# Kernel tuning notes

Measured on AMD Instinct MI355X. Metric: run time of the kernel, lower is better.

## Reference

```python
import jax, jax.numpy as jnp
import numpy as np

ALPHA = 0.2  # LeakyReLU slope
NEG = -1e9


def setup_inputs() -> dict:
    key = jax.random.key(0)
    k1, k2, k3, k4, k5 = jax.random.split(key, 5)
    B, N, F_IN, F_OUT, H = 8, 1024, 512, 256, 8
    x = jax.random.normal(k1, (B, N, F_IN), dtype=jnp.float32)
    adj = jax.random.randint(k2, (B, N, N), 0, 2, dtype=jnp.int32)
    W = jax.random.normal(k3, (H, F_OUT, F_IN), dtype=jnp.float32) * 0.05
    a1 = jax.random.normal(k4, (H, F_OUT), dtype=jnp.float32) * 0.05
    a2 = jax.random.normal(k5, (H, F_OUT), dtype=jnp.float32) * 0.05
    return {"x": x, "adj": adj, "W": W, "a1": a1, "a2": a2}


def _head(x, adj_zero, W, a1, a2):
    # x: (B,N,F_in), W: (F_out,F_in), a1/a2: (F_out,)
    h = jnp.einsum('bnf,of->bno', x, W)              # (B,N,F_out)
    f1 = jnp.einsum('bno,o->bn', h, a1)              # (B,N)
    f2 = jnp.einsum('bno,o->bn', h, a2)              # (B,N)
    e = f1[:, :, None] + f2[:, None, :]              # (B,N,N) broadcast add
    e = jax.nn.leaky_relu(e, negative_slope=ALPHA)
    e = jnp.where(adj_zero, NEG, e)                  # adjacency mask
    att = jax.nn.softmax(e, axis=2)
    return jnp.einsum('bnm,bmo->bno', att, h)        # (B,N,F_out)


def reference(x, adj, W, a1, a2):
    adj_zero = (adj == 0)
    # vmap over heads; sum of elu(head outputs)
    heads = jax.vmap(lambda w, u, v: _head(x, adj_zero, w, u, v))(W, a1, a2)  # (H,B,N,F_out)
    out = jnp.sum(jax.nn.elu(heads), axis=0)         # (B,N,F_out)
    return jax.nn.log_softmax(out, axis=2)
```

## Files before the change

### kernel.cpp

```cpp
#include <hip/hip_runtime.h>
#include <math.h>

#define B_    8
#define N_    1024
#define FIN   512
#define FOUT  256
#define H_    8
#define ALPHA 0.2f

#define XT (B_ * N_ * FIN)
#define WT (H_ * FOUT * FIN)

typedef short s16x8 __attribute__((ext_vector_type(8)));
typedef float f32x4 __attribute__((ext_vector_type(4)));

__device__ __forceinline__ unsigned short f2bf(float f) {
  unsigned int u = __float_as_uint(f);
  u = (u + 0x7FFFu + ((u >> 16) & 1u)) >> 16;
  return (unsigned short)u;
}

__device__ __forceinline__ unsigned int pk4_fp8(float a, float b, float c,
                                                float d) {
  int u = __builtin_amdgcn_cvt_pk_fp8_f32(a, b, 0, false);
  u = __builtin_amdgcn_cvt_pk_fp8_f32(c, d, u, true);
  return (unsigned int)u;
}

#if __has_builtin(__builtin_amdgcn_cvt_pk_f32_fp8)
#define HAVE_DEQ4 1
__device__ __forceinline__ float deq4(unsigned int u) {
  const auto a = __builtin_amdgcn_cvt_pk_f32_fp8((int)u, false);
  const auto b = __builtin_amdgcn_cvt_pk_f32_fp8((int)u, true);
  return (a[0] + a[1]) + (b[0] + b[1]);
}
#else
#define HAVE_DEQ4 0
__device__ __forceinline__ float q8e4m3(float p) {
  if (p >= 0.015625f) {
    unsigned int u = __float_as_uint(p);
    u = (u + 0x7FFFFu + ((u >> 20) & 1u)) & 0xFFF00000u;
    return __uint_as_float(u);
  }
  return (p + 16384.f) - 16384.f;
}
#endif

__device__ __forceinline__ void gload16(const void* g, void* l) {
  __builtin_amdgcn_global_load_lds(
      (const __attribute__((address_space(1))) unsigned int*)g,
      (__attribute__((address_space(3))) unsigned int*)l, 16, 0, 0);
}

__device__ __forceinline__ long gen8(unsigned int ab, const float4 fA,
                                     const float4 fB, float f1i, float mhat,
                                     float& dsum) {
  float ex[8];
#pragma unroll
  for (int j = 0; j < 8; ++j) {
    const float fv = j < 4 ? ((const float*)&fA)[j] : ((const float*)&fB)[j - 4];
    const float tt = f1i + fv;
    const float l = fmaxf(tt, ALPHA * tt);
    const float p = __expf(l - mhat);
    ex[j] = ((ab >> j) & 1u) ? p : 0.f;
  }
  const unsigned int lo = pk4_fp8(ex[0], ex[1], ex[2], ex[3]);
  const unsigned int hi = pk4_fp8(ex[4], ex[5], ex[6], ex[7]);
#if HAVE_DEQ4
  dsum += deq4(lo) + deq4(hi);
#else
#pragma unroll
  for (int j = 0; j < 8; ++j) dsum += q8e4m3(ex[j]);
#endif
  return (long)(((unsigned long long)hi << 32) | (unsigned long long)lo);
}


#define CVB  ((XT + WT) / 1024)
#define ZRB  128
#define PKB  ((B_ * N_ * 32) / 256)

__global__ __launch_bounds__(256) void prep(
    const float* __restrict__ x, const float* __restrict__ W,
    const int* __restrict__ adj, unsigned short* __restrict__ xb,
    unsigned short* __restrict__ Wb, float* __restrict__ f12,
    unsigned int* __restrict__ adjP) {
  const int blk = blockIdx.x;
  if (blk >= CVB + ZRB) {
    const int dw = (blk - CVB - ZRB) * 256 + threadIdx.x;
    const int r = dw >> 5, pd = dw & 31;
    const int q = pd >> 3, c8 = pd & 7;
    const int* ap = adj + (size_t)r * N_;
    unsigned int out = 0;
#pragma unroll
    for (int i = 0; i < 4; ++i) {
      const int jb = (c8 * 4 + i) * 32 + q * 8;
      int4 v0 = *(const int4*)(ap + jb);
      int4 v1 = *(const int4*)(ap + jb + 4);
      unsigned int byte = 0;
      byte |= (v0.x ? 1u : 0u) << 0; byte |= (v0.y ? 1u : 0u) << 1;
      byte |= (v0.z ? 1u : 0u) << 2; byte |= (v0.w ? 1u : 0u) << 3;
      byte |= (v1.x ? 1u : 0u) << 4; byte |= (v1.y ? 1u : 0u) << 5;
      byte |= (v1.z ? 1u : 0u) << 6; byte |= (v1.w ? 1u : 0u) << 7;
      out |= byte << (i * 8);
    }
    adjP[dw] = out;
    return;
  }
  if (blk >= CVB) {
    const int i = (blk - CVB) * 256 + threadIdx.x;
    ((float4*)f12)[i] = make_float4(0.f, 0.f, 0.f, 0.f);
    return;
  }
  const int i = (blk * 256 + threadIdx.x) * 4;
  const float* src;
  unsigned short* dst;
  int off;
  if (i < XT) { src = x; dst = xb; off = i; }
  else        { src = W; dst = Wb; off = i - XT; }
  float4 v = *(const float4*)(src + off);
  ushort4 s;
  s.x = f2bf(v.x); s.y = f2bf(v.y); s.z = f2bf(v.z); s.w = f2bf(v.w);
  *(ushort4*)(dst + off) = s;
}

__global__ __launch_bounds__(256, 3) void proj_mfma(
    const unsigned short* __restrict__ xb, const unsigned short* __restrict__ Wb,
    const float* __restrict__ a1, const float* __restrict__ a2,
    unsigned char* __restrict__ htq, float* __restrict__ f1,
    float* __restrict__ f2) {
  __shared__ __align__(16) unsigned short As[128 * 64];
  __shared__ __align__(16) unsigned short Bs[128 * 64];
  const int gid = blockIdx.x;
  const int b = gid & 7;
  const int mt_ = (gid >> 3) & 7;
  const int ot_ = (gid >> 6) & 1;
  const int h = gid >> 7;
  const int hb = h * B_ + b;
  const int m0 = mt_ * 128, o0 = ot_ * 128;
  const int t = threadIdx.x, w = t >> 6, lane = t & 63;
  const int col = lane & 15, quad = lane >> 4;

  const int srow = t >> 3;
  const int sseg = (t & 7) ^ (srow & 7);
  const unsigned short* agp = xb + (size_t)(b * N_ + m0 + srow) * FIN + sseg * 8;
  const unsigned short* bgp = Wb + (size_t)(h * FOUT + o0 + srow) * FIN + sseg * 8;

  f32x4 acc[2][8];
  const f32x4 z4 = {0.f, 0.f, 0.f, 0.f};
#pragma unroll
  for (int mt = 0; mt < 2; ++mt)
#pragma unroll
    for (int ot = 0; ot < 8; ++ot) acc[mt][ot] = z4;

  for (int it = 0; it < FIN / 64; ++it) {
    __syncthreads();
    const int k0 = it * 64;
#pragma unroll
    for (int i2 = 0; i2 < 4; ++i2) {
      gload16(agp + (size_t)i2 * 32 * FIN + k0, &As[i2 * 2048 + t * 8]);
      gload16(bgp + (size_t)i2 * 32 * FIN + k0, &Bs[i2 * 2048 + t * 8]);
    }
    __syncthreads();

#pragma unroll
    for (int kb = 0; kb < 2; ++kb) {
      s16x8 af[2], bf[8];
#pragma unroll
      for (int mt = 0; mt < 2; ++mt) {
        const int row = w * 32 + mt * 16 + col;
        af[mt] = *(const s16x8*)&As[row * 64 + ((kb * 4 + quad) ^ (row & 7)) * 8];
      }
#pragma unroll
      for (int ot = 0; ot < 8; ++ot) {
        const int row = ot * 16 + col;
        bf[ot] = *(const s16x8*)&Bs[row * 64 + ((kb * 4 + quad) ^ (row & 7)) * 8];
      }
#pragma unroll
      for (int mt = 0; mt < 2; ++mt)
#pragma unroll
        for (int ot = 0; ot < 8; ++ot)
          acc[mt][ot] = __builtin_amdgcn_mfma_f32_16x16x32_bf16(af[mt], bf[ot],
                                                                acc[mt][ot], 0, 0, 0);
    }
  }

  const int kkw = (m0 >> 5) + w;
  float pf1[2][4] = {{0.f}}, pf2[2][4] = {{0.f}};
#pragma unroll
  for (int mt = 0; mt < 2; ++mt) {
#pragma unroll
    for (int ot = 0; ot < 8; ++ot) {
      const int o = o0 + ot * 16 + col;
      const float va1 = a1[h * FOUT + o], va2 = a2[h * FOUT + o];
      const int otg = (o0 >> 4) + ot;
      unsigned char* fb =
          htq + (((size_t)(hb * 16 + otg) * 32 + kkw) << 9);
      const unsigned int q =
          pk4_fp8(acc[mt][ot][0], acc[mt][ot][1], acc[mt][ot][2], acc[mt][ot][3]);
      *(unsigned int*)(fb + (2 * mt + (quad >> 1)) * 128 + col * 8 +
                       (quad & 1) * 4) = q;
#pragma unroll
      for (int r = 0; r < 4; ++r) {
        pf1[mt][r] += acc[mt][ot][r] * va1;
        pf2[mt][r] += acc[mt][ot][r] * va2;
      }
    }
  }
#pragma unroll
  for (int off = 1; off <= 8; off <<= 1)
#pragma unroll
    for (int mt = 0; mt < 2; ++mt)
#pragma unroll
      for (int r = 0; r < 4; ++r) {
        pf1[mt][r] += __shfl_xor(pf1[mt][r], off);
        pf2[mt][r] += __shfl_xor(pf2[mt][r], off);
      }
  if (col == 0) {
#pragma unroll
    for (int mt = 0; mt < 2; ++mt)
#pragma unroll
      for (int r = 0; r < 4; ++r) {
        const int n = m0 + w * 32 + mt * 16 + quad * 4 + r;
        atomicAdd(&f1[hb * N_ + n], pf1[mt][r]);
        atomicAdd(&f2[hb * N_ + n], pf2[mt][r]);
      }
  }
}

__global__ __launch_bounds__(256, 4) void pv(
    const unsigned char* __restrict__ htq, const float* __restrict__ f1,
    const float* __restrict__ f2, const unsigned int* __restrict__ adjP,
    float* __restrict__ pp) {
  __shared__ __align__(16) unsigned char Bsh[2][16384];
  __shared__ __align__(16) float f2sh[N_];
  const int id = blockIdx.x;
  const int b = id & 7;
  const int oc = (id >> 3) & 1;
  const int h = (id >> 4) & 7;
  const int it = id >> 7;
  const int tid = threadIdx.x;
  const int w = tid >> 6, lane = tid & 63;
  const int col = lane & 15, quad = lane >> 4;
  const int rb = it * 8 + w * 2;

  const int hb = h * B_ + b;
  const unsigned char* bp = htq + (((size_t)(hb * 16 + oc * 8) * 32) << 9);
  const int row0 = rb * 16 + col;
  const int row1 = row0 + 16;
  const unsigned int* adp0 = adjP + ((size_t)(b * N_ + row0) << 5) + quad * 8;
  const unsigned int* adp1 = adjP + ((size_t)(b * N_ + row1) << 5) + quad * 8;

#define STAGE(buf, c)                                                        \
  {                                                                          \
    _Pragma("unroll")                                                        \
    for (int i = 0; i < 4; ++i) {                                            \
      const int flat = i * 4096 + tid * 16;                                  \
      gload16(bp + (size_t)(flat >> 11) * 16384 + (c) * 2048 + (flat & 2047),\
              &Bsh[buf][flat]);                                              \
    }                                                                        \
  }

  f32x4 acc[2][8];
  const f32x4 z4 = {0.f, 0.f, 0.f, 0.f};
#pragma unroll
  for (int g = 0; g < 2; ++g)
#pragma unroll
    for (int t = 0; t < 8; ++t) acc[g][t] = z4;

  const float* f2r = f2 + (size_t)hb * N_;
  gload16(f2r + tid * 4, &f2sh[tid * 4]);
  STAGE(0, 0)
  float m2 = -3.0e38f;
#pragma unroll
  for (int c = 0; c < 16; ++c) m2 = fmaxf(m2, f2r[lane + c * 64]);
#pragma unroll
  for (int off = 32; off; off >>= 1) m2 = fmaxf(m2, __shfl_xor(m2, off));
  const float f1a = f1[(size_t)hb * N_ + row0];
  const float f1b = f1[(size_t)hb * N_ + row1];
  const float tb0 = f1a + m2, tb1 = f1b + m2;
  const float mh0 = fmaxf(tb0, ALPHA * tb0);
  const float mh1 = fmaxf(tb1, ALPHA * tb1);
  unsigned int adA0 = adp0[0], adA1 = adp1[0];
  unsigned int adB0, adB1;
  float dsum0 = 0.f, dsum1 = 0.f;
  asm volatile("s_waitcnt vmcnt(0)" ::: "memory");
  __builtin_amdgcn_s_barrier();

#define PHASE(c, ADC0, ADC1, ADN0, ADN1)                                     \
  {                                                                          \
    if ((c) < 7) {                                                           \
      STAGE(1 - ((c) & 1), (c) + 1)                                          \
      ADN0 = adp0[(c) + 1];                                                  \
      ADN1 = adp1[(c) + 1];                                                  \
    }                                                                        \
    _Pragma("unroll")                                                        \
    for (int kkl = 0; kkl < 4; ++kkl) {                                      \
      const int kk = (c) * 4 + kkl;                                          \
      const float4 fA = *(const float4*)&f2sh[kk * 32 + quad * 8];           \
      const float4 fB = *(const float4*)&f2sh[kk * 32 + quad * 8 + 4];       \
      const long af0 =                                                       \
          gen8((ADC0 >> (kkl * 8)) & 0xFFu, fA, fB, f1a, mh0, dsum0);        \
      const long af1 =                                                       \
          gen8((ADC1 >> (kkl * 8)) & 0xFFu, fA, fB, f1b, mh1, dsum1);        \
      const unsigned char* bl_ = &Bsh[(c) & 1][kkl * 512 + lane * 8];        \
      __builtin_amdgcn_s_setprio(1);                                         \
      _Pragma("unroll")                                                      \
      for (int t = 0; t < 8; ++t) {                                          \
        const long bf = *(const long*)(bl_ + t * 2048);                      \
        acc[0][t] = __builtin_amdgcn_mfma_f32_16x16x32_fp8_fp8(af0, bf, acc[0][t], 0, 0, 0); \
        acc[1][t] = __builtin_amdgcn_mfma_f32_16x16x32_fp8_fp8(af1, bf, acc[1][t], 0, 0, 0); \
      }                                                                      \
      __builtin_amdgcn_s_setprio(0);                                         \
    }                                                                        \
    if ((c) < 7) {                                                           \
      asm volatile("s_waitcnt vmcnt(2)" ::: "memory");    \
      __builtin_amdgcn_s_barrier();                           \
    }                                                                        \
  }

  PHASE(0, adA0, adA1, adB0, adB1)
  PHASE(1, adB0, adB1, adA0, adA1)
  PHASE(2, adA0, adA1, adB0, adB1)
  PHASE(3, adB0, adB1, adA0, adA1)
  PHASE(4, adA0, adA1, adB0, adB1)
  PHASE(5, adB0, adB1, adA0, adA1)
  PHASE(6, adA0, adA1, adB0, adB1)
  PHASE(7, adB0, adB1, adA0, adA1)
#undef PHASE
#undef STAGE

  dsum0 += __shfl_xor(dsum0, 16);
  dsum0 += __shfl_xor(dsum0, 32);
  dsum1 += __shfl_xor(dsum1, 16);
  dsum1 += __shfl_xor(dsum1, 32);

  float* pdst = pp + (size_t)h * ((size_t)B_ * N_ * FOUT);
#pragma unroll
  for (int g = 0; g < 2; ++g)
#pragma unroll
    for (int r = 0; r < 4; ++r) {
      const float den = __shfl(g == 0 ? dsum0 : dsum1, quad * 4 + r);
      const float inv = 1.0f / den;
      const int orow = (rb + g) * 16 + quad * 4 + r;
#pragma unroll
      for (int t = 0; t < 8; ++t) {
        const float oh = acc[g][t][r] * inv;
        pdst[(size_t)(b * N_ + orow) * FOUT + oc * 128 + t * 16 + col] =
            oh > 0.f ? oh : __expf(oh) - 1.f;
      }
    }
}

__global__ __launch_bounds__(256) void logsm(
    const float* __restrict__ pp, float* __restrict__ out) {
  const int row = blockIdx.x * 4 + (threadIdx.x >> 6);
  const int lane = threadIdx.x & 63;
  const size_t base = (size_t)row * FOUT;
  const size_t PSZ = (size_t)B_ * N_ * FOUT;
  float v[4];
  float m = -3.0e38f;
#pragma unroll
  for (int c = 0; c < 4; ++c) {
    const size_t idx = base + c * 64 + lane;
    float s = 0.f;
#pragma unroll
    for (int hh = 0; hh < 8; ++hh) s += pp[hh * PSZ + idx];
    v[c] = s;
    m = fmaxf(m, v[c]);
  }
#pragma unroll
  for (int off = 32; off; off >>= 1) m = fmaxf(m, __shfl_xor(m, off));
  float s = 0.f;
#pragma unroll
  for (int c = 0; c < 4; ++c) s += __expf(v[c] - m);
#pragma unroll
  for (int off = 32; off; off >>= 1) s += __shfl_xor(s, off);
  const float lg = m + logf(s);
#pragma unroll
  for (int c = 0; c < 4; ++c)
    out[base + c * 64 + lane] = v[c] - lg;
}

extern "C" void kernel_launch(void* const* d_in, const int* in_sizes, int n_in,
                              void* d_out, int out_size, void* d_ws,
                              size_t ws_size, hipStream_t stream) {
  const float* x   = (const float*)d_in[0];
  const int*   adj = (const int*)d_in[1];
  const float* W   = (const float*)d_in[2];
  const float* a1  = (const float*)d_in[3];
  const float* a2  = (const float*)d_in[4];
  float* out = (float*)d_out;

  unsigned char* htq = (unsigned char*)d_ws;
  unsigned short* xb = (unsigned short*)(htq + (size_t)H_ * B_ * FOUT * N_);
  unsigned short* Wb = xb + (size_t)XT;
  float* f1 = (float*)(Wb + (size_t)WT);
  float* f2 = f1 + (size_t)H_ * B_ * N_;
  float* pad = f2 + (size_t)H_ * B_ * N_;
  float* part2 = pad + (size_t)H_ * B_ * N_;
  float* part3 = part2 + (size_t)B_ * N_ * FOUT;
  unsigned int* adjP = (unsigned int*)(part3 + (size_t)B_ * N_ * FOUT);
  float* pp = (float*)(adjP + (size_t)B_ * N_ * 32);

  prep<<<CVB + ZRB + PKB, 256, 0, stream>>>(x, W, adj, xb, Wb, f1, adjP);

  proj_mfma<<<1024, 256, 0, stream>>>(xb, Wb, a1, a2, htq, f1, f2);

  pv<<<1024, 256, 0, stream>>>(htq, f1, f2, adjP, pp);

  logsm<<<(B_ * N_) / 4, 256, 0, stream>>>(pp, out);
}
```

Before: 214.5 us.

## Software-pipeline attention fragment generation one phase ahead of MFMA in pv

Each phase of the pv kernel now builds the fp8 attention A-fragments for the next phase while it issues MFMAs on fragments precomputed in the previous phase, using double-buffered register arrays. All adjacency words are loaded up front with vector loads instead of one per phase, and the per-phase wait becomes vmcnt(0). Launch bounds drop from 4 to 3 waves per EU so the extra registers fit. The aim is to overlap the VALU exp and pack work with matrix-core execution, at the cost of lower occupancy and a stricter memory wait.

```diff
diff --git a/kernel.cpp b/kernel.cpp
--- a/kernel.cpp
+++ b/kernel.cpp
@@ -228,7 +228,7 @@
   }
 }
 
-__global__ __launch_bounds__(256, 4) void pv(
+__global__ __launch_bounds__(256, 3) void pv(
     const unsigned char* __restrict__ htq, const float* __restrict__ f1,
     const float* __restrict__ f2, const unsigned int* __restrict__ adjP,
     float* __restrict__ pp) {
@@ -271,6 +271,15 @@
   const float* f2r = f2 + (size_t)hb * N_;
   gload16(f2r + tid * 4, &f2sh[tid * 4]);
   STAGE(0, 0)
+  const uint4 av00 = *(const uint4*)(adp0);
+  const uint4 av01 = *(const uint4*)(adp0 + 4);
+  const uint4 av10 = *(const uint4*)(adp1);
+  const uint4 av11 = *(const uint4*)(adp1 + 4);
+  unsigned int a0[8], a1[8];
+  a0[0] = av00.x; a0[1] = av00.y; a0[2] = av00.z; a0[3] = av00.w;
+  a0[4] = av01.x; a0[5] = av01.y; a0[6] = av01.z; a0[7] = av01.w;
+  a1[0] = av10.x; a1[1] = av10.y; a1[2] = av10.z; a1[3] = av10.w;
+  a1[4] = av11.x; a1[5] = av11.y; a1[6] = av11.z; a1[7] = av11.w;
   float m2 = -3.0e38f;
 #pragma unroll
   for (int c = 0; c < 16; ++c) m2 = fmaxf(m2, f2r[lane + c * 64]);
@@ -281,52 +290,57 @@
   const float tb0 = f1a + m2, tb1 = f1b + m2;
   const float mh0 = fmaxf(tb0, ALPHA * tb0);
   const float mh1 = fmaxf(tb1, ALPHA * tb1);
-  unsigned int adA0 = adp0[0], adA1 = adp1[0];
-  unsigned int adB0, adB1;
   float dsum0 = 0.f, dsum1 = 0.f;
   asm volatile("s_waitcnt vmcnt(0)" ::: "memory");
   __builtin_amdgcn_s_barrier();
 
-#define PHASE(c, ADC0, ADC1, ADN0, ADN1)                                     \
+  long Ae[8], Ao[8];
+#pragma unroll
+  for (int kkl = 0; kkl < 4; ++kkl) {
+    const float4 fA = *(const float4*)&f2sh[kkl * 32 + quad * 8];
+    const float4 fB = *(const float4*)&f2sh[kkl * 32 + quad * 8 + 4];
+    Ae[kkl] = gen8((a0[0] >> (kkl * 8)) & 0xFFu, fA, fB, f1a, mh0, dsum0);
+    Ae[4 + kkl] = gen8((a1[0] >> (kkl * 8)) & 0xFFu, fA, fB, f1b, mh1, dsum1);
+  }
+
+#define PHASE(c, Acur, Anxt)                                                 \
   {                                                                          \
-    if ((c) < 7) {                                                           \
-      STAGE(1 - ((c) & 1), (c) + 1)                                          \
-      ADN0 = adp0[(c) + 1];                                                  \
-      ADN1 = adp1[(c) + 1];                                                  \
-    }                                                                        \
+    if ((c) < 7) STAGE(1 - ((c) & 1), (c) + 1)                               \
     _Pragma("unroll")                                                        \
     for (int kkl = 0; kkl < 4; ++kkl) {                                      \
-      const int kk = (c) * 4 + kkl;                                          \
-      const float4 fA = *(const float4*)&f2sh[kk * 32 + quad * 8];           \
-      const float4 fB = *(const float4*)&f2sh[kk * 32 + quad * 8 + 4];       \
-      const long af0 =                                                       \
-          gen8((ADC0 >> (kkl * 8)) & 0xFFu, fA, fB, f1a, mh0, dsum0);        \
-      const long af1 =                                                       \
-          gen8((ADC1 >> (kkl * 8)) & 0xFFu, fA, fB, f1b, mh1, dsum1);        \
+      if ((c) < 7) {  \
+        const int kk = ((c) + 1) * 4 + kkl;      \
+        const float4 fA = *(const float4*)&f2sh[kk * 32 + quad * 8];         \
+        const float4 fB = *(const float4*)&f2sh[kk * 32 + quad * 8 + 4];     \
+        Anxt[kkl] =                                                          \
+            gen8((a0[(c) + 1] >> (kkl * 8)) & 0xFFu, fA, fB, f1a, mh0, dsum0); \
+        Anxt[4 + kkl] =                                                      \
+            gen8((a1[(c) + 1] >> (kkl * 8)) & 0xFFu, fA, fB, f1b, mh1, dsum1); \
+      }                                                                      \
       const unsigned char* bl_ = &Bsh[(c) & 1][kkl * 512 + lane * 8];        \
       __builtin_amdgcn_s_setprio(1);                                         \
       _Pragma("unroll")                                                      \
       for (int t = 0; t < 8; ++t) {                                          \
         const long bf = *(const long*)(bl_ + t * 2048);                      \
-        acc[0][t] = __builtin_amdgcn_mfma_f32_16x16x32_fp8_fp8(af0, bf, acc[0][t], 0, 0, 0); \
-        acc[1][t] = __builtin_amdgcn_mfma_f32_16x16x32_fp8_fp8(af1, bf, acc[1][t], 0, 0, 0); \
+        acc[0][t] = __builtin_amdgcn_mfma_f32_16x16x32_fp8_fp8(Acur[kkl], bf, acc[0][t], 0, 0, 0); \
+        acc[1][t] = __builtin_amdgcn_mfma_f32_16x16x32_fp8_fp8(Acur[4 + kkl], bf, acc[1][t], 0, 0, 0); \
       }                                                                      \
       __builtin_amdgcn_s_setprio(0);                                         \
     }                                                                        \
     if ((c) < 7) {                                                           \
-      asm volatile("s_waitcnt vmcnt(2)" ::: "memory");    \
-      __builtin_amdgcn_s_barrier();                           \
+      asm volatile("s_waitcnt vmcnt(0)" ::: "memory"); \
+      __builtin_amdgcn_s_barrier();                                          \
     }                                                                        \
   }
 
-  PHASE(0, adA0, adA1, adB0, adB1)
-  PHASE(1, adB0, adB1, adA0, adA1)
-  PHASE(2, adA0, adA1, adB0, adB1)
-  PHASE(3, adB0, adB1, adA0, adA1)
-  PHASE(4, adA0, adA1, adB0, adB1)
-  PHASE(5, adB0, adB1, adA0, adA1)
-  PHASE(6, adA0, adA1, adB0, adB1)
-  PHASE(7, adB0, adB1, adA0, adA1)
+  PHASE(0, Ae, Ao)
+  PHASE(1, Ao, Ae)
+  PHASE(2, Ae, Ao)
+  PHASE(3, Ao, Ae)
+  PHASE(4, Ae, Ao)
+  PHASE(5, Ao, Ae)
+  PHASE(6, Ae, Ao)
+  PHASE(7, Ao, Ae)
 #undef PHASE
 #undef STAGE
 
```

Result: faster. 203.5 us (-5.1%).
